# Optimization experiments

Hardware: AMD Instinct MI355X
Metric: run time of the kernel (lower is better)

## Reference

```python
import jax, jax.numpy as jnp
import numpy as np

N_NODES = 50000
N_EDGES = 1600000  # even; edges come in reverse pairs (i, i^1)
D_NODE = 128
D_EDGE = 32
UNITS = 128
STEPS = 4


def setup_inputs() -> dict:
    key = jax.random.key(0)
    ks = jax.random.split(key, 8)
    # Build directed edges as adjacent reverse pairs so rev(e) = e XOR 1.
    half = N_EDGES // 2
    src = jax.random.randint(ks[0], (half,), 0, N_NODES, dtype=jnp.int32)
    dst = jax.random.randint(ks[1], (half,), 0, N_NODES, dtype=jnp.int32)
    edge_src = jnp.stack([src, dst], axis=1).reshape(-1)
    edge_dst = jnp.stack([dst, src], axis=1).reshape(-1)
    node_feature = jax.random.normal(ks[2], (N_NODES, D_NODE), dtype=jnp.float32)
    edge_feature = jax.random.normal(ks[3], (N_EDGES, D_EDGE), dtype=jnp.float32)
    s_i = 1.0 / np.sqrt(D_NODE + D_EDGE)
    s_u = 1.0 / np.sqrt(UNITS)
    s_f = 1.0 / np.sqrt(D_NODE + UNITS)
    Wi = jax.random.normal(ks[4], (D_NODE + D_EDGE, UNITS), dtype=jnp.float32) * s_i
    Wu = jax.random.normal(ks[5], (UNITS, UNITS), dtype=jnp.float32) * s_u
    Wf = jax.random.normal(ks[6], (D_NODE + UNITS, UNITS), dtype=jnp.float32) * s_f
    bi = jnp.zeros((UNITS,), jnp.float32)
    bu = jnp.zeros((UNITS,), jnp.float32)
    bf = jnp.zeros((UNITS,), jnp.float32)
    return {
        'node_feature': node_feature, 'edge_feature': edge_feature,
        'edge_src': edge_src, 'edge_dst': edge_dst,
        'Wi': Wi, 'bi': bi, 'Wu': Wu, 'bu': bu, 'Wf': Wf, 'bf': bf,
    }


def reference(node_feature, edge_feature, edge_src, edge_dst, Wi, bi, Wu, bu, Wf, bf):
    n_nodes = node_feature.shape[0]
    n_edges = edge_src.shape[0]
    # reverse edge of e is e XOR 1 (edges built as adjacent pairs)
    rev = jnp.bitwise_xor(jnp.arange(n_edges, dtype=jnp.int32), 1)

    # initial projection: relu([x_src || e] Wi + bi)  -> [E, UNITS]
    h = jax.nn.relu(
        jnp.concatenate([node_feature[edge_src], edge_feature], axis=-1) @ Wi + bi)

    for _ in range(STEPS):
        # aggregate incoming edge states at each node, gather at edge_src,
        # subtract the reverse edge state (DMPNN message)
        agg = jax.ops.segment_sum(h, edge_dst, num_segments=n_nodes)  # [N, UNITS]
        message = agg[edge_src] - h[rev]                              # [E, UNITS]
        h = jax.nn.relu(message @ Wu + bu + h)

    node_message = jax.ops.segment_sum(h, edge_dst, num_segments=n_nodes)
    out = jax.nn.relu(
        jnp.concatenate([node_feature, node_message], axis=-1) @ Wf + bf)
    return out
```

## Files before the change

kernel.cpp:

```cpp
#include <hip/hip_runtime.h>
#include <hip/hip_bf16.h>

#define N_NODES 50000
#define N_EDGES 1600000
#define TILE    128

typedef __bf16 bf16x8 __attribute__((ext_vector_type(8)));
typedef float  f32x4  __attribute__((ext_vector_type(4)));

static __device__ __forceinline__ bf16x8 ld8(const __bf16* p) {
  return *reinterpret_cast<const bf16x8*>(p);
}
static __device__ __forceinline__ void st8(__bf16* p, bf16x8 v) {
  *reinterpret_cast<bf16x8*>(p) = v;
}

static __device__ __forceinline__ void async16(const void* g, void* l) {
  auto gp = (const __attribute__((address_space(1))) unsigned int*)(unsigned long long)g;
  auto lp = (__attribute__((address_space(3))) unsigned int*)(unsigned int)(unsigned long long)l;
  __builtin_amdgcn_global_load_lds(gp, lp, 16, 0, 0);
}

__global__ __launch_bounds__(256) void k_prep_w(
    const float* __restrict__ Wi, const float* __restrict__ Wu,
    const float* __restrict__ Wf,
    __bf16* __restrict__ WiT, __bf16* __restrict__ WuT, __bf16* __restrict__ WfT)
{
  int g = blockIdx.x * 256 + threadIdx.x;
  if (g < 160 * 128) {
    int n = g / 160, k = g % 160;
    WiT[g] = (__bf16)Wi[k * 128 + n];
  } else if (g < 160 * 128 + 128 * 128) {
    int gg = g - 160 * 128;
    int n = gg / 128, k = gg % 128;
    WuT[gg] = (__bf16)Wu[k * 128 + n];
  } else if (g < 160 * 128 + 128 * 128 + 256 * 128) {
    int gg = g - (160 * 128 + 128 * 128);
    int n = gg / 256, k = gg % 256;
    WfT[gg] = (__bf16)Wf[k * 128 + n];
  }
}

__global__ __launch_bounds__(256) void k_cvt(
    const float* __restrict__ in, __bf16* __restrict__ out, long n)
{
  long i = ((long)blockIdx.x * 256 + threadIdx.x) * 8;
  if (i + 8 <= n) {
    f32x4 f0 = *(const f32x4*)(in + i);
    f32x4 f1 = *(const f32x4*)(in + i + 4);
    bf16x8 o;
#pragma unroll
    for (int j = 0; j < 4; ++j) { o[j] = (__bf16)f0[j]; o[4 + j] = (__bf16)f1[j]; }
    st8(out + i, o);
  }
}

__global__ __launch_bounds__(256) void k_hist(
    const int* __restrict__ edst, int* __restrict__ cnt)
{
  int e = blockIdx.x * 256 + threadIdx.x;
  if (e < N_EDGES) atomicAdd(&cnt[edst[e]], 1);
}

__global__ __launch_bounds__(1024) void k_scan1(
    int* __restrict__ cnt, int* __restrict__ bsum, int n)
{
  __shared__ int sm[1024];
  const int tid = threadIdx.x;
  int i = blockIdx.x * 1024 + tid;
  int v = (i < n) ? cnt[i] : 0;
  sm[tid] = v;
  __syncthreads();
  for (int off = 1; off < 1024; off <<= 1) {
    int t = (tid >= off) ? sm[tid - off] : 0;
    __syncthreads();
    sm[tid] += t;
    __syncthreads();
  }
  if (i < n) cnt[i] = sm[tid] - v;
  if (tid == 1023) bsum[blockIdx.x] = sm[1023];
}

__global__ __launch_bounds__(64) void k_scan2(int* __restrict__ bsum, int nb)
{
  if (threadIdx.x == 0) {
    int acc = 0;
    for (int k = 0; k < nb; ++k) { int t = bsum[k]; bsum[k] = acc; acc += t; }
  }
}

__global__ __launch_bounds__(256) void k_scan3(
    const int* __restrict__ cnt, const int* __restrict__ bsum,
    int* __restrict__ cursor, int n)
{
  int i = blockIdx.x * 256 + threadIdx.x;
  if (i < n) cursor[i] = cnt[i] + bsum[i >> 10];
}

__global__ __launch_bounds__(256) void k_fill(
    const int* __restrict__ edst, int* __restrict__ cursor, int* __restrict__ eidx)
{
  int e = blockIdx.x * 256 + threadIdx.x;
  if (e < N_EDGES) {
    int p = atomicAdd(&cursor[edst[e]], 1);
    eidx[p] = e;
  }
}

__global__ __launch_bounds__(256) void k_agg(
    const __bf16* __restrict__ h, const int* __restrict__ cnt,
    const int* __restrict__ bsum, const int* __restrict__ eidx,
    __bf16* __restrict__ aggbf)
{
  const int wave = threadIdx.x >> 6;
  const int node = blockIdx.x * 4 + wave;
  const int lane = threadIdx.x & 63;
  const int g = lane >> 3, c8 = lane & 7;
  const int s = cnt[node] + bsum[node >> 10];
  const int e = (node + 1 < N_NODES) ? (cnt[node + 1] + bsum[(node + 1) >> 10]) : N_EDGES;
  const int deg = e - s;

  float a[16] = {};
  if (deg > 0) {
    const int* bucket = eidx + s;
    const int nit = (deg + 7) >> 3;
    int j0 = g;
    int e0 = bucket[(j0 < deg) ? j0 : 0];
    int e1 = bucket[(j0 + 8 < deg) ? j0 + 8 : 0];
    bool v0 = (j0 < deg), v1 = (j0 + 8 < deg);
    for (int it = 0; it < nit; ++it) {
      const int j2 = j0 + 16;
      const int e2 = bucket[(j2 < deg) ? j2 : 0];
      const __bf16* hp = h + (long)e0 * 128 + c8 * 16;
      bf16x8 r0 = ld8(hp), r1 = ld8(hp + 8);
#pragma unroll
      for (int k = 0; k < 8; ++k) {
        a[k]     += v0 ? (float)r0[k] : 0.f;
        a[8 + k] += v0 ? (float)r1[k] : 0.f;
      }
      e0 = e1; v0 = v1;
      e1 = e2; v1 = (j2 < deg);
      j0 += 8;
    }
  }
#pragma unroll
  for (int k = 0; k < 16; ++k) {
    a[k] += __shfl_xor(a[k], 8, 64);
    a[k] += __shfl_xor(a[k], 16, 64);
    a[k] += __shfl_xor(a[k], 32, 64);
  }
  if (g == 0) {
    bf16x8 o0, o1;
#pragma unroll
    for (int k = 0; k < 8; ++k) { o0[k] = (__bf16)a[k]; o1[k] = (__bf16)a[8 + k]; }
    st8(aggbf + (long)node * 128 + c8 * 16, o0);
    st8(aggbf + (long)node * 128 + c8 * 16 + 8, o1);
  }
}

__global__ __launch_bounds__(256) void k_nodegemm(
    const __bf16* __restrict__ A, const __bf16* __restrict__ BT, const int ldb,
    const float* __restrict__ bias, __bf16* __restrict__ outb, const int nrows)
{
  const int tid = threadIdx.x;
  const int lane = tid & 63, wave = tid >> 6;
  const int l15 = lane & 15, quad = lane >> 4;
  const int wm = wave >> 1, wn = wave & 1;
  const int base = blockIdx.x * TILE;

  int rowm[4];
#pragma unroll
  for (int ms = 0; ms < 4; ++ms) {
    int nd = base + wm * 64 + ms * 16 + l15;
    rowm[ms] = nd < nrows ? nd : (nrows - 1);
  }
  f32x4 acc[4][4] = {};
#pragma unroll
  for (int kit = 0; kit < 4; ++kit) {
    const int koff = kit * 32 + quad * 8;
    bf16x8 a[4];
#pragma unroll
    for (int ms = 0; ms < 4; ++ms)
      a[ms] = ld8(A + (long)rowm[ms] * 128 + koff);
#pragma unroll
    for (int ns = 0; ns < 4; ++ns) {
      bf16x8 b = ld8(BT + (wn * 64 + ns * 16 + l15) * ldb + koff);
#pragma unroll
      for (int ms = 0; ms < 4; ++ms)
        acc[ms][ns] = __builtin_amdgcn_mfma_f32_16x16x32_bf16(a[ms], b, acc[ms][ns], 0, 0, 0);
    }
  }
#pragma unroll
  for (int ns = 0; ns < 4; ++ns) {
    const int col = wn * 64 + ns * 16 + l15;
    const float bv = bias[col];
#pragma unroll
    for (int ms = 0; ms < 4; ++ms) {
      const int r0 = wm * 64 + ms * 16 + quad * 4;
#pragma unroll
      for (int r = 0; r < 4; ++r) {
        const int node = base + r0 + r;
        if (node < nrows) outb[(long)node * 128 + col] = (__bf16)(acc[ms][ns][r] + bv);
      }
    }
  }
}

__global__ __launch_bounds__(256) void k_init(
    const float* __restrict__ ef, const int* __restrict__ esrc,
    const __bf16* __restrict__ WiT, const __bf16* __restrict__ q,
    __bf16* __restrict__ h)
{
  __shared__ __align__(16) char smem[32768];
  float*  efT  = (float*)smem;
  __bf16* cbuf = (__bf16*)smem;
  const int tid = threadIdx.x;
  const int lane = tid & 63, wave = tid >> 6;
  const int l15 = lane & 15, quad = lane >> 4;
  const int wm = wave >> 1, wn = wave & 1;
  const long base = (long)blockIdx.x * TILE;

#pragma unroll
  for (int j = 0; j < 4; ++j) {
    const int r = wave * 32 + j * 8 + (lane >> 3);
    const int cd = (lane & 7) ^ (r & 7);
    async16(ef + (base + r) * 32 + cd * 4, efT + (wave * 32 + j * 8) * 32);
  }
  __syncthreads();

  f32x4 acc[4][4] = {};
  {
    bf16x8 a[4];
#pragma unroll
    for (int ms = 0; ms < 4; ++ms) {
      const int rm = wm * 64 + ms * 16 + l15;
      const int c0 = (quad * 2) ^ (rm & 7);
      f32x4 f0 = *(const f32x4*)(efT + rm * 32 + c0 * 4);
      f32x4 f1 = *(const f32x4*)(efT + rm * 32 + (c0 ^ 1) * 4);
      bf16x8 v;
#pragma unroll
      for (int j = 0; j < 4; ++j) { v[j] = (__bf16)f0[j]; v[4 + j] = (__bf16)f1[j]; }
      a[ms] = v;
    }
#pragma unroll
    for (int ns = 0; ns < 4; ++ns) {
      bf16x8 b = ld8(WiT + (wn * 64 + ns * 16 + l15) * 160 + 128 + quad * 8);
#pragma unroll
      for (int ms = 0; ms < 4; ++ms)
        acc[ms][ns] = __builtin_amdgcn_mfma_f32_16x16x32_bf16(a[ms], b, acc[ms][ns], 0, 0, 0);
    }
  }

  const int c15 = tid & 15, rbase = tid >> 4;
  int srcv[8];
#pragma unroll
  for (int i = 0; i < 8; ++i) srcv[i] = esrc[base + i * 16 + rbase];
  bf16x8 gp0 = ld8(q + (long)srcv[0] * 128 + c15 * 8);
  bf16x8 gp1 = ld8(q + (long)srcv[1] * 128 + c15 * 8);

  __syncthreads();
#pragma unroll
  for (int ns = 0; ns < 4; ++ns) {
    const int col = wn * 64 + ns * 16 + l15;
#pragma unroll
    for (int ms = 0; ms < 4; ++ms) {
      const int r0 = wm * 64 + ms * 16 + quad * 4;
#pragma unroll
      for (int r = 0; r < 4; ++r) {
        const int row = r0 + r;
        cbuf[row * 128 + (((col >> 3) ^ (row & 15)) * 8) + (col & 7)] = (__bf16)acc[ms][ns][r];
      }
    }
  }
  __syncthreads();

#pragma unroll
  for (int i = 0; i < 8; ++i) {
    bf16x8 gnext;
    if (i < 6) gnext = ld8(q + (long)srcv[i + 2] * 128 + c15 * 8);
    const int row = i * 16 + rbase;
    bf16x8 cv = ld8(cbuf + row * 128 + ((c15 ^ (row & 15)) * 8));
    bf16x8 o;
#pragma unroll
    for (int j = 0; j < 8; ++j) {
      float v = (float)gp0[j] + (float)cv[j];
      v = v > 0.f ? v : 0.f;
      o[j] = (__bf16)v;
    }
    st8(h + (base + row) * 128 + c15 * 8, o);
    gp0 = gp1; gp1 = gnext;
  }
}

__global__ __launch_bounds__(256) void k_update(
    __bf16* __restrict__ h, const int* __restrict__ esrc,
    const __bf16* __restrict__ WuT, const __bf16* __restrict__ gW)
{
  __shared__ __align__(16) __bf16 smem[128 * 128];
  const int tid = threadIdx.x;
  const int lane = tid & 63, wave = tid >> 6;
  const int l15 = lane & 15, quad = lane >> 4;
  const int wm = wave >> 1, wn = wave & 1;
  const long base = (long)blockIdx.x * TILE;

#pragma unroll
  for (int j = 0; j < 8; ++j) {
    const int r = wave * 32 + j * 4 + (lane >> 4);
    const int cd = (lane & 15) ^ (r & 15);
    async16(h + (base + r) * 128 + cd * 8, smem + (wave * 32 + j * 4) * 128);
  }
  __syncthreads();

  f32x4 acc[4][4] = {};
#pragma unroll
  for (int kit = 0; kit < 4; ++kit) {
    bf16x8 a[4];
#pragma unroll
    for (int ms = 0; ms < 4; ++ms) {
      const int rm = wm * 64 + ms * 16 + l15;
      a[ms] = ld8(smem + rm * 128 + (((kit * 4 + quad) ^ l15) * 8));
    }
#pragma unroll
    for (int ns = 0; ns < 4; ++ns) {
      bf16x8 b = ld8(WuT + (wn * 64 + ns * 16 + l15) * 128 + kit * 32 + quad * 8);
#pragma unroll
      for (int ms = 0; ms < 4; ++ms)
        acc[ms][ns] = __builtin_amdgcn_mfma_f32_16x16x32_bf16(a[ms], b, acc[ms][ns], 0, 0, 0);
    }
  }

  const int c15 = tid & 15, rbase = tid >> 4;
  bf16x8 hv[8];
  int srcv[8];
#pragma unroll
  for (int i = 0; i < 8; ++i) {
    const int row = i * 16 + rbase;
    hv[i] = ld8(smem + row * 128 + ((c15 ^ (row & 15)) * 8));
    srcv[i] = esrc[base + row];
  }
  bf16x8 gp0 = ld8(gW + (long)srcv[0] * 128 + c15 * 8);
  bf16x8 gp1 = ld8(gW + (long)srcv[1] * 128 + c15 * 8);

  __syncthreads();
#pragma unroll
  for (int ns = 0; ns < 4; ++ns) {
    const int col = wn * 64 + ns * 16 + l15;
#pragma unroll
    for (int ms = 0; ms < 4; ++ms) {
      const int r0 = wm * 64 + ms * 16 + quad * 4;
#pragma unroll
      for (int r = 0; r < 4; ++r) {
        const int row = r0 + r;
        smem[row * 128 + (((col >> 3) ^ (row & 15)) * 8) + (col & 7)] = (__bf16)acc[ms][ns][r];
      }
    }
  }
  __syncthreads();

#pragma unroll
  for (int i = 0; i < 8; ++i) {
    bf16x8 gnext;
    if (i < 6) gnext = ld8(gW + (long)srcv[i + 2] * 128 + c15 * 8);
    const int row = i * 16 + rbase;
    const int rowr = row ^ 1;
    bf16x8 cv = ld8(smem + rowr * 128 + ((c15 ^ (rowr & 15)) * 8));
    bf16x8 o;
#pragma unroll
    for (int j = 0; j < 8; ++j) {
      float v = (float)gp0[j] - (float)cv[j] + (float)hv[i][j];
      v = v > 0.f ? v : 0.f;
      o[j] = (__bf16)v;
    }
    st8(h + (base + row) * 128 + c15 * 8, o);
    gp0 = gp1; gp1 = gnext;
  }
}

__global__ __launch_bounds__(256) void k_final(
    const __bf16* __restrict__ nfbf, const __bf16* __restrict__ aggbf,
    const __bf16* __restrict__ WfT, const float* __restrict__ bfb,
    float* __restrict__ out)
{
  const int tid = threadIdx.x;
  const int lane = tid & 63, wave = tid >> 6;
  const int l15 = lane & 15, quad = lane >> 4;
  const int wm = wave >> 1, wn = wave & 1;
  const int base = blockIdx.x * TILE;

  int nodem[4];
#pragma unroll
  for (int ms = 0; ms < 4; ++ms) {
    int nd = base + wm * 64 + ms * 16 + l15;
    nodem[ms] = nd < N_NODES ? nd : (N_NODES - 1);
  }
  f32x4 acc[4][4] = {};
#pragma unroll
  for (int kit = 0; kit < 8; ++kit) {
    const int koff = kit * 32 + quad * 8;
    bf16x8 a[4];
#pragma unroll
    for (int ms = 0; ms < 4; ++ms)
      a[ms] = (kit < 4) ? ld8(nfbf + (long)nodem[ms] * 128 + koff)
                        : ld8(aggbf + (long)nodem[ms] * 128 + (koff - 128));
#pragma unroll
    for (int ns = 0; ns < 4; ++ns) {
      bf16x8 b = ld8(WfT + (wn * 64 + ns * 16 + l15) * 256 + koff);
#pragma unroll
      for (int ms = 0; ms < 4; ++ms)
        acc[ms][ns] = __builtin_amdgcn_mfma_f32_16x16x32_bf16(a[ms], b, acc[ms][ns], 0, 0, 0);
    }
  }
#pragma unroll
  for (int ns = 0; ns < 4; ++ns) {
    const int col = wn * 64 + ns * 16 + l15;
    const float bias = bfb[col];
#pragma unroll
    for (int ms = 0; ms < 4; ++ms) {
      const int r0 = wm * 64 + ms * 16 + quad * 4;
#pragma unroll
      for (int r = 0; r < 4; ++r) {
        const int node = base + r0 + r;
        if (node < N_NODES) {
          float v = acc[ms][ns][r] + bias;
          out[(long)node * 128 + col] = v > 0.f ? v : 0.f;
        }
      }
    }
  }
}

extern "C" void kernel_launch(void* const* d_in, const int* in_sizes, int n_in,
                              void* d_out, int out_size, void* d_ws, size_t ws_size,
                              hipStream_t stream) {
  const float* nf   = (const float*)d_in[0];
  const float* ef   = (const float*)d_in[1];
  const int*   esrc = (const int*)d_in[2];
  const int*   edst = (const int*)d_in[3];
  const float* Wi   = (const float*)d_in[4];
  const float* bi   = (const float*)d_in[5];
  const float* Wu   = (const float*)d_in[6];
  const float* bu   = (const float*)d_in[7];
  const float* Wf   = (const float*)d_in[8];
  const float* bfb  = (const float*)d_in[9];
  float* out = (float*)d_out;

  char* ws = (char*)d_ws;
  __bf16* h      = (__bf16*)(ws);
  __bf16* aggbf  = (__bf16*)(ws + 409600000L);
  __bf16* nfbf   = (__bf16*)(ws + 422400000L);
  __bf16* WiT    = (__bf16*)(ws + 435200000L);
  __bf16* WuT    = (__bf16*)(ws + 435240960L);
  __bf16* WfT    = (__bf16*)(ws + 435273728L);
  int*    cnt    = (int*)(ws + 435339264L);
  int*    cursor = (int*)(ws + 435539264L);
  int*    bsum   = (int*)(ws + 435739264L);
  int*    eidx   = (int*)(ws + 435739520L);
  __bf16* g      = (__bf16*)(ws + 442139520L);

  const long NV = (long)N_NODES * 128;
  const int  NGB = (N_NODES + TILE - 1) / TILE;

  hipLaunchKernelGGL(k_prep_w, dim3(272), dim3(256), 0, stream, Wi, Wu, Wf, WiT, WuT, WfT);
  hipLaunchKernelGGL(k_cvt, dim3(3125), dim3(256), 0, stream, nf, nfbf, NV);
  hipMemsetAsync(cnt, 0, 200000, stream);
  hipLaunchKernelGGL(k_hist, dim3(N_EDGES / 256), dim3(256), 0, stream, edst, cnt);
  hipLaunchKernelGGL(k_scan1, dim3(49), dim3(1024), 0, stream, cnt, bsum, N_NODES);
  hipLaunchKernelGGL(k_scan2, dim3(1), dim3(64), 0, stream, bsum, 49);
  hipLaunchKernelGGL(k_scan3, dim3(196), dim3(256), 0, stream, cnt, bsum, cursor, N_NODES);
  hipLaunchKernelGGL(k_fill, dim3(N_EDGES / 256), dim3(256), 0, stream, edst, cursor, eidx);

  hipLaunchKernelGGL(k_nodegemm, dim3(NGB), dim3(256), 0, stream, nfbf, WiT, 160, bi, g, N_NODES);
  hipLaunchKernelGGL(k_init, dim3(N_EDGES / TILE), dim3(256), 0, stream, ef, esrc, WiT, g, h);

  for (int t = 0; t < 4; ++t) {
    hipLaunchKernelGGL(k_agg, dim3(N_NODES / 4), dim3(256), 0, stream, h, cnt, bsum, eidx, aggbf);
    hipLaunchKernelGGL(k_nodegemm, dim3(NGB), dim3(256), 0, stream, aggbf, WuT, 128, bu, g, N_NODES);
    hipLaunchKernelGGL(k_update, dim3(N_EDGES / TILE), dim3(256), 0, stream, h, esrc, WuT, g);
  }
  hipLaunchKernelGGL(k_agg, dim3(N_NODES / 4), dim3(256), 0, stream, h, cnt, bsum, eidx, aggbf);
  hipLaunchKernelGGL(k_final, dim3(NGB), dim3(256), 0, stream, nfbf, aggbf, WfT, bfb, out);
}
```

Baseline: 2.169 ms.

## Swap MFMA operands for row-contiguous outputs and drop LDS epilogue round-trip

The MFMA operands are swapped (weights as A, activations as B), so each lane holds four consecutive output columns of one row. That lets the epilogues write bf16x4/f32x4 vectors directly, with no per-element scatter or LDS staging. k_update now gets the reverse-edge term with a lane shuffle (xor 1), replacing a second LDS pass and barrier. The gathers of the source-node rows are issued before the first barrier, and k_init/k_update move to 512-thread blocks with 8 waves each owning 32 rows. The cost is narrower 8-byte stores and gathers and changed register pressure under the launch bound of 512 threads with a minimum of 4 blocks.

```diff
diff --git a/kernel.cpp b/kernel.cpp
--- a/kernel.cpp
+++ b/kernel.cpp
@@ -6,6 +6,7 @@
 #define TILE    128
 
 typedef __bf16 bf16x8 __attribute__((ext_vector_type(8)));
+typedef __bf16 bf16x4 __attribute__((ext_vector_type(4)));
 typedef float  f32x4  __attribute__((ext_vector_type(4)));
 
 static __device__ __forceinline__ bf16x8 ld8(const __bf16* p) {
@@ -178,42 +179,41 @@
 #pragma unroll
   for (int kit = 0; kit < 4; ++kit) {
     const int koff = kit * 32 + quad * 8;
-    bf16x8 a[4];
+    bf16x8 b[4];
 #pragma unroll
     for (int ms = 0; ms < 4; ++ms)
-      a[ms] = ld8(A + (long)rowm[ms] * 128 + koff);
+      b[ms] = ld8(A + (long)rowm[ms] * 128 + koff);
 #pragma unroll
     for (int ns = 0; ns < 4; ++ns) {
-      bf16x8 b = ld8(BT + (wn * 64 + ns * 16 + l15) * ldb + koff);
+      bf16x8 a = ld8(BT + (wn * 64 + ns * 16 + l15) * ldb + koff);
 #pragma unroll
       for (int ms = 0; ms < 4; ++ms)
-        acc[ms][ns] = __builtin_amdgcn_mfma_f32_16x16x32_bf16(a[ms], b, acc[ms][ns], 0, 0, 0);
+        acc[ms][ns] = __builtin_amdgcn_mfma_f32_16x16x32_bf16(a, b[ms], acc[ms][ns], 0, 0, 0);
     }
   }
 #pragma unroll
   for (int ns = 0; ns < 4; ++ns) {
-    const int col = wn * 64 + ns * 16 + l15;
-    const float bv = bias[col];
+    const int col = wn * 64 + ns * 16 + quad * 4;
+    const f32x4 bv = *(const f32x4*)(bias + col);
 #pragma unroll
     for (int ms = 0; ms < 4; ++ms) {
-      const int r0 = wm * 64 + ms * 16 + quad * 4;
-#pragma unroll
-      for (int r = 0; r < 4; ++r) {
-        const int node = base + r0 + r;
-        if (node < nrows) outb[(long)node * 128 + col] = (__bf16)(acc[ms][ns][r] + bv);
+      const int node = base + wm * 64 + ms * 16 + l15;
+      if (node < nrows) {
+        bf16x4 o;
+#pragma unroll
+        for (int j = 0; j < 4; ++j) o[j] = (__bf16)(acc[ms][ns][j] + bv[j]);
+        *(bf16x4*)(outb + (long)node * 128 + col) = o;
       }
     }
   }
 }
 
-__global__ __launch_bounds__(256) void k_init(
+__global__ __launch_bounds__(512, 4) void k_init(
     const float* __restrict__ ef, const int* __restrict__ esrc,
     const __bf16* __restrict__ WiT, const __bf16* __restrict__ q,
     __bf16* __restrict__ h)
 {
-  __shared__ __align__(16) char smem[32768];
-  float*  efT  = (float*)smem;
-  __bf16* cbuf = (__bf16*)smem;
+  __shared__ __align__(16) float efT[128 * 32];
   const int tid = threadIdx.x;
   const int lane = tid & 63, wave = tid >> 6;
   const int l15 = lane & 15, quad = lane >> 4;
@@ -221,78 +221,62 @@
   const long base = (long)blockIdx.x * TILE;
 
 #pragma unroll
-  for (int j = 0; j < 4; ++j) {
-    const int r = wave * 32 + j * 8 + (lane >> 3);
+  for (int j = 0; j < 2; ++j) {
+    const int r = wave * 16 + j * 8 + (lane >> 3);
     const int cd = (lane & 7) ^ (r & 7);
-    async16(ef + (base + r) * 32 + cd * 4, efT + (wave * 32 + j * 8) * 32);
-  }
+    async16(ef + (base + r) * 32 + cd * 4, efT + (wave * 16 + j * 8) * 32);
+  }
+
+  int srcv[2];
+#pragma unroll
+  for (int ms = 0; ms < 2; ++ms) srcv[ms] = esrc[base + wm * 32 + ms * 16 + l15];
+  bf16x4 gp[2][4];
+#pragma unroll
+  for (int ms = 0; ms < 2; ++ms)
+#pragma unroll
+    for (int ns = 0; ns < 4; ++ns)
+      gp[ms][ns] = *(const bf16x4*)(q + (long)srcv[ms] * 128 + wn * 64 + ns * 16 + quad * 4);
+
   __syncthreads();
 
-  f32x4 acc[4][4] = {};
-  {
-    bf16x8 a[4];
-#pragma unroll
-    for (int ms = 0; ms < 4; ++ms) {
-      const int rm = wm * 64 + ms * 16 + l15;
-      const int c0 = (quad * 2) ^ (rm & 7);
-      f32x4 f0 = *(const f32x4*)(efT + rm * 32 + c0 * 4);
-      f32x4 f1 = *(const f32x4*)(efT + rm * 32 + (c0 ^ 1) * 4);
-      bf16x8 v;
-#pragma unroll
-      for (int j = 0; j < 4; ++j) { v[j] = (__bf16)f0[j]; v[4 + j] = (__bf16)f1[j]; }
-      a[ms] = v;
-    }
+  f32x4 acc[2][4] = {};
+  bf16x8 b[2];
+#pragma unroll
+  for (int ms = 0; ms < 2; ++ms) {
+    const int rm = wm * 32 + ms * 16 + l15;
+    const int c0 = (quad * 2) ^ (rm & 7);
+    f32x4 f0 = *(const f32x4*)(efT + rm * 32 + c0 * 4);
+    f32x4 f1 = *(const f32x4*)(efT + rm * 32 + (c0 ^ 1) * 4);
+    bf16x8 v;
+#pragma unroll
+    for (int j = 0; j < 4; ++j) { v[j] = (__bf16)f0[j]; v[4 + j] = (__bf16)f1[j]; }
+    b[ms] = v;
+  }
+#pragma unroll
+  for (int ns = 0; ns < 4; ++ns) {
+    bf16x8 a = ld8(WiT + (wn * 64 + ns * 16 + l15) * 160 + 128 + quad * 8);
+#pragma unroll
+    for (int ms = 0; ms < 2; ++ms)
+      acc[ms][ns] = __builtin_amdgcn_mfma_f32_16x16x32_bf16(a, b[ms], acc[ms][ns], 0, 0, 0);
+  }
+
+#pragma unroll
+  for (int ms = 0; ms < 2; ++ms) {
+    const int rloc = wm * 32 + ms * 16 + l15;
 #pragma unroll
     for (int ns = 0; ns < 4; ++ns) {
-      bf16x8 b = ld8(WiT + (wn * 64 + ns * 16 + l15) * 160 + 128 + quad * 8);
-#pragma unroll
-      for (int ms = 0; ms < 4; ++ms)
-        acc[ms][ns] = __builtin_amdgcn_mfma_f32_16x16x32_bf16(a[ms], b, acc[ms][ns], 0, 0, 0);
-    }
-  }
-
-  const int c15 = tid & 15, rbase = tid >> 4;
-  int srcv[8];
-#pragma unroll
-  for (int i = 0; i < 8; ++i) srcv[i] = esrc[base + i * 16 + rbase];
-  bf16x8 gp0 = ld8(q + (long)srcv[0] * 128 + c15 * 8);
-  bf16x8 gp1 = ld8(q + (long)srcv[1] * 128 + c15 * 8);
-
-  __syncthreads();
-#pragma unroll
-  for (int ns = 0; ns < 4; ++ns) {
-    const int col = wn * 64 + ns * 16 + l15;
-#pragma unroll
-    for (int ms = 0; ms < 4; ++ms) {
-      const int r0 = wm * 64 + ms * 16 + quad * 4;
-#pragma unroll
-      for (int r = 0; r < 4; ++r) {
-        const int row = r0 + r;
-        cbuf[row * 128 + (((col >> 3) ^ (row & 15)) * 8) + (col & 7)] = (__bf16)acc[ms][ns][r];
+      bf16x4 o;
+#pragma unroll
+      for (int j = 0; j < 4; ++j) {
+        float v = (float)gp[ms][ns][j] + acc[ms][ns][j];
+        o[j] = (__bf16)(v > 0.f ? v : 0.f);
       }
-    }
-  }
-  __syncthreads();
-
-#pragma unroll
-  for (int i = 0; i < 8; ++i) {
-    bf16x8 gnext;
-    if (i < 6) gnext = ld8(q + (long)srcv[i + 2] * 128 + c15 * 8);
-    const int row = i * 16 + rbase;
-    bf16x8 cv = ld8(cbuf + row * 128 + ((c15 ^ (row & 15)) * 8));
-    bf16x8 o;
-#pragma unroll
-    for (int j = 0; j < 8; ++j) {
-      float v = (float)gp0[j] + (float)cv[j];
-      v = v > 0.f ? v : 0.f;
-      o[j] = (__bf16)v;
-    }
-    st8(h + (base + row) * 128 + c15 * 8, o);
-    gp0 = gp1; gp1 = gnext;
-  }
-}
-
-__global__ __launch_bounds__(256) void k_update(
+      *(bf16x4*)(h + (base + rloc) * 128 + wn * 64 + ns * 16 + quad * 4) = o;
+    }
+  }
+}
+
+__global__ __launch_bounds__(512, 4) void k_update(
     __bf16* __restrict__ h, const int* __restrict__ esrc,
     const __bf16* __restrict__ WuT, const __bf16* __restrict__ gW)
 {
@@ -304,75 +288,61 @@
   const long base = (long)blockIdx.x * TILE;
 
 #pragma unroll
-  for (int j = 0; j < 8; ++j) {
-    const int r = wave * 32 + j * 4 + (lane >> 4);
+  for (int j = 0; j < 4; ++j) {
+    const int r = wave * 16 + j * 4 + (lane >> 4);
     const int cd = (lane & 15) ^ (r & 15);
-    async16(h + (base + r) * 128 + cd * 8, smem + (wave * 32 + j * 4) * 128);
-  }
+    async16(h + (base + r) * 128 + cd * 8, smem + (wave * 16 + j * 4) * 128);
+  }
+
+  int srcv[2];
+#pragma unroll
+  for (int ms = 0; ms < 2; ++ms) srcv[ms] = esrc[base + wm * 32 + ms * 16 + l15];
+  bf16x4 gp[2][4];
+#pragma unroll
+  for (int ms = 0; ms < 2; ++ms)
+#pragma unroll
+    for (int ns = 0; ns < 4; ++ns)
+      gp[ms][ns] = *(const bf16x4*)(gW + (long)srcv[ms] * 128 + wn * 64 + ns * 16 + quad * 4);
+
   __syncthreads();
 
-  f32x4 acc[4][4] = {};
+  f32x4 acc[2][4] = {};
 #pragma unroll
   for (int kit = 0; kit < 4; ++kit) {
-    bf16x8 a[4];
-#pragma unroll
-    for (int ms = 0; ms < 4; ++ms) {
-      const int rm = wm * 64 + ms * 16 + l15;
-      a[ms] = ld8(smem + rm * 128 + (((kit * 4 + quad) ^ l15) * 8));
+    bf16x8 b[2];
+#pragma unroll
+    for (int ms = 0; ms < 2; ++ms) {
+      const int rm = wm * 32 + ms * 16 + l15;
+      b[ms] = ld8(smem + rm * 128 + (((kit * 4 + quad) ^ l15) * 8));
     }
 #pragma unroll
     for (int ns = 0; ns < 4; ++ns) {
-      bf16x8 b = ld8(WuT + (wn * 64 + ns * 16 + l15) * 128 + kit * 32 + quad * 8);
-#pragma unroll
-      for (int ms = 0; ms < 4; ++ms)
-        acc[ms][ns] = __builtin_amdgcn_mfma_f32_16x16x32_bf16(a[ms], b, acc[ms][ns], 0, 0, 0);
-    }
-  }
-
-  const int c15 = tid & 15, rbase = tid >> 4;
-  bf16x8 hv[8];
-  int srcv[8];
-#pragma unroll
-  for (int i = 0; i < 8; ++i) {
-    const int row = i * 16 + rbase;
-    hv[i] = ld8(smem + row * 128 + ((c15 ^ (row & 15)) * 8));
-    srcv[i] = esrc[base + row];
-  }
-  bf16x8 gp0 = ld8(gW + (long)srcv[0] * 128 + c15 * 8);
-  bf16x8 gp1 = ld8(gW + (long)srcv[1] * 128 + c15 * 8);
-
-  __syncthreads();
-#pragma unroll
-  for (int ns = 0; ns < 4; ++ns) {
-    const int col = wn * 64 + ns * 16 + l15;
-#pragma unroll
-    for (int ms = 0; ms < 4; ++ms) {
-      const int r0 = wm * 64 + ms * 16 + quad * 4;
-#pragma unroll
-      for (int r = 0; r < 4; ++r) {
-        const int row = r0 + r;
-        smem[row * 128 + (((col >> 3) ^ (row & 15)) * 8) + (col & 7)] = (__bf16)acc[ms][ns][r];
+      bf16x8 a = ld8(WuT + (wn * 64 + ns * 16 + l15) * 128 + kit * 32 + quad * 8);
+#pragma unroll
+      for (int ms = 0; ms < 2; ++ms)
+        acc[ms][ns] = __builtin_amdgcn_mfma_f32_16x16x32_bf16(a, b[ms], acc[ms][ns], 0, 0, 0);
+    }
+  }
+
+#pragma unroll
+  for (int ms = 0; ms < 2; ++ms) {
+    const int rloc = wm * 32 + ms * 16 + l15;
+#pragma unroll
+    for (int ns = 0; ns < 4; ++ns) {
+      const int c8g = wn * 8 + ns * 2 + (quad >> 1);
+      const __bf16* rp = smem + rloc * 128 + ((c8g ^ l15) * 8) + (quad & 1) * 4;
+      bf16x4 hr = *(const bf16x4*)rp;
+      f32x4 rv;
+#pragma unroll
+      for (int j = 0; j < 4; ++j) rv[j] = __shfl_xor(acc[ms][ns][j], 1, 64);
+      bf16x4 o;
+#pragma unroll
+      for (int j = 0; j < 4; ++j) {
+        float v = (float)gp[ms][ns][j] - rv[j] + (float)hr[j];
+        o[j] = (__bf16)(v > 0.f ? v : 0.f);
       }
-    }
-  }
-  __syncthreads();
-
-#pragma unroll
-  for (int i = 0; i < 8; ++i) {
-    bf16x8 gnext;
-    if (i < 6) gnext = ld8(gW + (long)srcv[i + 2] * 128 + c15 * 8);
-    const int row = i * 16 + rbase;
-    const int rowr = row ^ 1;
-    bf16x8 cv = ld8(smem + rowr * 128 + ((c15 ^ (rowr & 15)) * 8));
-    bf16x8 o;
-#pragma unroll
-    for (int j = 0; j < 8; ++j) {
-      float v = (float)gp0[j] - (float)cv[j] + (float)hv[i][j];
-      v = v > 0.f ? v : 0.f;
-      o[j] = (__bf16)v;
-    }
-    st8(h + (base + row) * 128 + c15 * 8, o);
-    gp0 = gp1; gp1 = gnext;
+      *(bf16x4*)(h + (base + rloc) * 128 + wn * 64 + ns * 16 + quad * 4) = o;
+    }
   }
 }
 
@@ -387,43 +357,44 @@
   const int wm = wave >> 1, wn = wave & 1;
   const int base = blockIdx.x * TILE;
 
-  int nodem[4];
+  int rowm[4];
 #pragma unroll
   for (int ms = 0; ms < 4; ++ms) {
     int nd = base + wm * 64 + ms * 16 + l15;
-    nodem[ms] = nd < N_NODES ? nd : (N_NODES - 1);
+    rowm[ms] = nd < N_NODES ? nd : (N_NODES - 1);
   }
   f32x4 acc[4][4] = {};
 #pragma unroll
   for (int kit = 0; kit < 8; ++kit) {
     const int koff = kit * 32 + quad * 8;
-    bf16x8 a[4];
+    bf16x8 b[4];
 #pragma unroll
     for (int ms = 0; ms < 4; ++ms)
-      a[ms] = (kit < 4) ? ld8(nfbf + (long)nodem[ms] * 128 + koff)
-                        : ld8(aggbf + (long)nodem[ms] * 128 + (koff - 128));
+      b[ms] = (kit < 4) ? ld8(nfbf + (long)rowm[ms] * 128 + koff)
+                        : ld8(aggbf + (long)rowm[ms] * 128 + (koff - 128));
 #pragma unroll
     for (int ns = 0; ns < 4; ++ns) {
-      bf16x8 b = ld8(WfT + (wn * 64 + ns * 16 + l15) * 256 + koff);
+      bf16x8 a = ld8(WfT + (wn * 64 + ns * 16 + l15) * 256 + koff);
 #pragma unroll
       for (int ms = 0; ms < 4; ++ms)
-        acc[ms][ns] = __builtin_amdgcn_mfma_f32_16x16x32_bf16(a[ms], b, acc[ms][ns], 0, 0, 0);
+        acc[ms][ns] = __builtin_amdgcn_mfma_f32_16x16x32_bf16(a, b[ms], acc[ms][ns], 0, 0, 0);
     }
   }
 #pragma unroll
   for (int ns = 0; ns < 4; ++ns) {
-    const int col = wn * 64 + ns * 16 + l15;
-    const float bias = bfb[col];
+    const int col = wn * 64 + ns * 16 + quad * 4;
+    const f32x4 bv = *(const f32x4*)(bfb + col);
 #pragma unroll
     for (int ms = 0; ms < 4; ++ms) {
-      const int r0 = wm * 64 + ms * 16 + quad * 4;
-#pragma unroll
-      for (int r = 0; r < 4; ++r) {
-        const int node = base + r0 + r;
-        if (node < N_NODES) {
-          float v = acc[ms][ns][r] + bias;
-          out[(long)node * 128 + col] = v > 0.f ? v : 0.f;
+      const int node = base + wm * 64 + ms * 16 + l15;
+      if (node < N_NODES) {
+        f32x4 o;
+#pragma unroll
+        for (int j = 0; j < 4; ++j) {
+          float v = acc[ms][ns][j] + bv[j];
+          o[j] = v > 0.f ? v : 0.f;
         }
+        *(f32x4*)(out + (long)node * 128 + col) = o;
       }
     }
   }
@@ -470,12 +441,12 @@
   hipLaunchKernelGGL(k_fill, dim3(N_EDGES / 256), dim3(256), 0, stream, edst, cursor, eidx);
 
   hipLaunchKernelGGL(k_nodegemm, dim3(NGB), dim3(256), 0, stream, nfbf, WiT, 160, bi, g, N_NODES);
-  hipLaunchKernelGGL(k_init, dim3(N_EDGES / TILE), dim3(256), 0, stream, ef, esrc, WiT, g, h);
+  hipLaunchKernelGGL(k_init, dim3(N_EDGES / TILE), dim3(512), 0, stream, ef, esrc, WiT, g, h);
 
   for (int t = 0; t < 4; ++t) {
     hipLaunchKernelGGL(k_agg, dim3(N_NODES / 4), dim3(256), 0, stream, h, cnt, bsum, eidx, aggbf);
     hipLaunchKernelGGL(k_nodegemm, dim3(NGB), dim3(256), 0, stream, aggbf, WuT, 128, bu, g, N_NODES);
-    hipLaunchKernelGGL(k_update, dim3(N_EDGES / TILE), dim3(256), 0, stream, h, esrc, WuT, g);
+    hipLaunchKernelGGL(k_update, dim3(N_EDGES / TILE), dim3(512), 0, stream, h, esrc, WuT, g);
   }
   hipLaunchKernelGGL(k_agg, dim3(N_NODES / 4), dim3(256), 0, stream, h, cnt, bsum, eidx, aggbf);
   hipLaunchKernelGGL(k_final, dim3(NGB), dim3(256), 0, stream, nfbf, aggbf, WfT, bfb, out);
```

Result: slower. 2.826 ms (+30.3%).
